# Kernel tuning notes

Measured on AMD Instinct MI355X. Metric: run time of the kernel, lower is better.

## Reference

```python
import jax, jax.numpy as jnp
import numpy as np


def setup_inputs() -> dict:
    key = jax.random.key(0)
    k1, k2 = jax.random.split(key)
    B, S, H, D = 2, 2048, 16, 64
    qk = jax.random.normal(k1, (B, S, 2, H, D), dtype=jnp.float32)
    v = jax.random.normal(k2, (B, S, H, D), dtype=jnp.float32)
    return {"qk": qk, "v": v}


def reference(qk, v):
    # qk: (B, S, 2, H, D); v: (B, S, H, D)
    seqlen = qk.shape[1]
    q = qk[:, :, 0]  # (B, S, H, D)
    k = qk[:, :, 1]
    # elu(x) + 1 feature map (positive features)
    q = jax.nn.elu(q) + 1.0
    k = jax.nn.elu(k) + 1.0
    # explicit O(S^2) score matrix: (B, H, T, S)
    scores = jnp.einsum('bthd,bshd->bhts', q, k)
    mask = jnp.tril(jnp.ones((seqlen, seqlen), dtype=scores.dtype))
    scores = scores * mask
    nu = scores.sum(axis=-1)  # (B, H, T)
    attention = scores / nu[:, :, :, None]
    # dropout_p = 0.0 (eval mode): identity
    output = jnp.einsum('bhts,bshd->bthd', attention, v)
    return output
```

## Files before the change

kernel.cpp:

```cpp
#include <hip/hip_runtime.h>


#define BB 2
#define SS 2048
#define HH 16
#define DD 64
#define CC 128
#define NC (SS / CC)
#define BH (BB * HH)
#define NCHUNK (BH * NC)

#define ST_STRIDE 8448LL
#define WS_KB (512LL * ST_STRIDE)
#define WS_VT (WS_KB + 512LL * 16384)
#define WS_S0 (WS_VT + 512LL * 16384)
#define WS_KZ (WS_S0 + 512LL * 8192)

typedef __attribute__((ext_vector_type(8))) short bf16x8;
typedef __attribute__((ext_vector_type(4))) float f32x4;

__device__ __forceinline__ float phi(float x) {
    return x > 0.f ? x + 1.f : __expf(x);
}
__device__ __forceinline__ unsigned short f2bf(float x) {
    unsigned int u = __float_as_uint(x);
    u += 0x7fffu + ((u >> 16) & 1u);
    return (unsigned short)(u >> 16);
}
__device__ __forceinline__ float bf2f(unsigned short b) {
    return __uint_as_float(((unsigned int)b) << 16);
}
__device__ __forceinline__ void gload16(const void* g, void* lds) {
    __builtin_amdgcn_global_load_lds(
        (const __attribute__((address_space(1))) unsigned int*)g,
        (__attribute__((address_space(3))) unsigned int*)lds, 16, 0, 0);
}

__global__ __launch_bounds__(256, 2)
void prep_state(const float* __restrict__ qk, const float* __restrict__ v,
                char* __restrict__ st, unsigned short* __restrict__ kbg,
                unsigned short* __restrict__ vtg) {
    __shared__ unsigned short Kt[DD][136];
    __shared__ unsigned short Vt[DD][136];

    const int tid = threadIdx.x, blk = blockIdx.x;
    const int bh = blk / NC, c = blk % NC, b = bh / HH, h = bh % HH;
    const int s0 = c * CC;
    const int lr = tid >> 4, lc = (tid & 15) * 4;
    char* kbc = (char*)kbg + (size_t)blk * 16384;

    #pragma unroll
    for (int it = 0; it < 8; ++it) {
        int row = it * 16 + lr;
        size_t ka = ((size_t)((b * SS + s0 + row) * 2 + 1)) * (HH * DD) + h * DD + lc;
        float4 kv = *(const float4*)(qk + ka);
        ushort4 kq = make_ushort4(f2bf(phi(kv.x)), f2bf(phi(kv.y)),
                                  f2bf(phi(kv.z)), f2bf(phi(kv.w)));
        *(ushort4*)(kbc + row * 128 + ((lc * 2) ^ ((row & 7) << 4))) = kq;
        Kt[lc + 0][row] = kq.x; Kt[lc + 1][row] = kq.y;
        Kt[lc + 2][row] = kq.z; Kt[lc + 3][row] = kq.w;
        size_t va = ((size_t)((b * SS + s0 + row) * HH + h)) * DD + lc;
        float4 vv = *(const float4*)(v + va);
        Vt[lc + 0][row] = f2bf(vv.x); Vt[lc + 1][row] = f2bf(vv.y);
        Vt[lc + 2][row] = f2bf(vv.z); Vt[lc + 3][row] = f2bf(vv.w);
    }
    __syncthreads();

    {
        char* vtc = (char*)vtg + (size_t)blk * 16384;
        int e = tid >> 2, sq = (tid & 3) * 32;
        #pragma unroll
        for (int k8 = 0; k8 < 4; ++k8) {
            int s = sq + k8 * 8;
            bf16x8 val = *(const bf16x8*)&Vt[e][s];
            *(bf16x8*)(vtc + e * 256 + ((s * 2) ^ ((e & 7) << 4))) = val;
        }
    }

    const int w = tid >> 6, lane = tid & 63, g = lane >> 4, ln = lane & 15;
    {
        bf16x8 av[4];
        #pragma unroll
        for (int ks = 0; ks < 4; ++ks)
            av[ks] = *(const bf16x8*)&Vt[w * 16 + ln][ks * 32 + g * 8];
        bf16x8 ones;
        #pragma unroll
        for (int j = 0; j < 8; ++j) ones[j] = (short)0x3F80;

        char* stc = st + (size_t)blk * ST_STRIDE;
        #pragma unroll
        for (int n = 0; n < 4; ++n) {
            f32x4 a = {0.f, 0.f, 0.f, 0.f}, kz4 = {0.f, 0.f, 0.f, 0.f};
            #pragma unroll
            for (int ks = 0; ks < 4; ++ks) {
                bf16x8 bk = *(const bf16x8*)&Kt[n * 16 + ln][ks * 32 + g * 8];
                a = __builtin_amdgcn_mfma_f32_16x16x32_bf16(av[ks], bk, a, 0, 0, 0);
                if (w == 0)
                    kz4 = __builtin_amdgcn_mfma_f32_16x16x32_bf16(ones, bk, kz4, 0, 0, 0);
            }
            #pragma unroll
            for (int r = 0; r < 4; ++r)
                *(unsigned short*)(stc + (((w * 16 + g * 4 + r) * 64) + n * 16 + ln) * 2)
                    = f2bf(a[r]);
            if (w == 0 && g == 0)
                *(float*)(stc + 8192 + (n * 16 + ln) * 4) = kz4[0];
        }
    }
}

__global__ __launch_bounds__(256)
void chunk_scan(const char* __restrict__ st, unsigned short* __restrict__ s0g,
                float* __restrict__ kzg) {
    int flat = blockIdx.x * 256 + threadIdx.x;
    int bh = flat / 1040, i = flat % 1040;
    const char* stb = st + (size_t)(bh * NC) * ST_STRIDE;
    if (i < 1024) {
        int i4 = i * 4, e = i4 >> 6, d = i4 & 63;
        const char* src = stb + i * 8;
        char* dst = (char*)s0g + (size_t)(bh * NC) * 8192
                    + e * 128 + ((d * 2) ^ ((e & 7) << 4));
        float4 run = {0.f, 0.f, 0.f, 0.f};
        #pragma unroll
        for (int c2 = 0; c2 < NC; ++c2) {
            *(ushort4*)(dst + (size_t)c2 * 8192) =
                make_ushort4(f2bf(run.x), f2bf(run.y), f2bf(run.z), f2bf(run.w));
            ushort4 x = *(const ushort4*)(src + (size_t)c2 * ST_STRIDE);
            run.x += bf2f(x.x); run.y += bf2f(x.y);
            run.z += bf2f(x.z); run.w += bf2f(x.w);
        }
    } else {
        int j = (i - 1024) * 4;
        const char* src = stb + 8192 + j * 4;
        float* dst = kzg + (size_t)(bh * NC) * 64 + j;
        float4 run = {0.f, 0.f, 0.f, 0.f};
        #pragma unroll
        for (int c2 = 0; c2 < NC; ++c2) {
            *(float4*)(dst + (size_t)c2 * 64) = run;
            float4 x = *(const float4*)(src + (size_t)c2 * ST_STRIDE);
            run.x += x.x; run.y += x.y; run.z += x.z; run.w += x.w;
        }
    }
}

__global__ __launch_bounds__(256, 2)
void lin_attn_out(const float* __restrict__ qk,
                  const unsigned short* __restrict__ kbg,
                  const unsigned short* __restrict__ vtg,
                  const unsigned short* __restrict__ s0g,
                  const float* __restrict__ kzg,
                  float* __restrict__ out) {
    __shared__ __align__(16) char KbL[16384];
    __shared__ __align__(16) char VtL[16384];
    __shared__ __align__(16) char S0L[8192];
    __shared__ float kzl[DD];
    __shared__ __align__(16) unsigned short Wl[4][32][40];
    __shared__ float nul[4][32];

    const int tid = threadIdx.x, blk = blockIdx.x;
    const int bh = blk / NC, c = blk % NC, b = bh / HH, h = bh % HH;
    const int s0 = c * CC;
    const int w = tid >> 6, lane = tid & 63, g = lane >> 4, ln = lane & 15;
    const int wband = (blk & 1) ? (3 - w) : w;

    {
        const char* kbs = (const char*)kbg + (size_t)blk * 16384;
        const char* vts = (const char*)vtg + (size_t)blk * 16384;
        const char* s0s = (const char*)s0g + (size_t)blk * 8192;
        #pragma unroll
        for (int i = 0; i < 4; ++i) {
            gload16(kbs + w * 4096 + i * 1024 + lane * 16, KbL + w * 4096 + i * 1024);
            gload16(vts + w * 4096 + i * 1024 + lane * 16, VtL + w * 4096 + i * 1024);
        }
        #pragma unroll
        for (int i = 0; i < 2; ++i)
            gload16(s0s + w * 2048 + i * 1024 + lane * 16, S0L + w * 2048 + i * 1024);
        if (tid < DD) kzl[tid] = kzg[(size_t)blk * 64 + tid];
    }

    bf16x8 aq[2][2];
    #pragma unroll
    for (int m = 0; m < 2; ++m) {
        int tg = s0 + wband * 32 + m * 16 + ln;
        const float* qrow = qk + ((size_t)((b * SS + tg) * 2)) * (HH * DD) + h * DD;
        #pragma unroll
        for (int kb2 = 0; kb2 < 2; ++kb2) {
            float4 x0 = *(const float4*)(qrow + kb2 * 32 + g * 8);
            float4 x1 = *(const float4*)(qrow + kb2 * 32 + g * 8 + 4);
            bf16x8 f;
            f[0] = (short)f2bf(phi(x0.x)); f[1] = (short)f2bf(phi(x0.y));
            f[2] = (short)f2bf(phi(x0.z)); f[3] = (short)f2bf(phi(x0.w));
            f[4] = (short)f2bf(phi(x1.x)); f[5] = (short)f2bf(phi(x1.y));
            f[6] = (short)f2bf(phi(x1.z)); f[7] = (short)f2bf(phi(x1.w));
            aq[m][kb2] = f;
        }
    }
    __syncthreads();

    f32x4 O[2][4];
    #pragma unroll
    for (int m = 0; m < 2; ++m)
        #pragma unroll
        for (int n = 0; n < 4; ++n) O[m][n] = (f32x4){0.f, 0.f, 0.f, 0.f};

    #pragma unroll
    for (int n = 0; n < 4; ++n) {
        int e = n * 16 + ln;
        bf16x8 b0 = *(const bf16x8*)(S0L + e * 128 + ((g * 16) ^ ((e & 7) << 4)));
        bf16x8 b1 = *(const bf16x8*)(S0L + e * 128 + ((64 + g * 16) ^ ((e & 7) << 4)));
        #pragma unroll
        for (int m = 0; m < 2; ++m) {
            O[m][n] = __builtin_amdgcn_mfma_f32_16x16x32_bf16(aq[m][0], b0, O[m][n], 0, 0, 0);
            O[m][n] = __builtin_amdgcn_mfma_f32_16x16x32_bf16(aq[m][1], b1, O[m][n], 0, 0, 0);
        }
    }

    float nuA[2] = {0.f, 0.f};
    #pragma unroll
    for (int kb2 = 0; kb2 < 2; ++kb2)
        #pragma unroll
        for (int j = 0; j < 8; ++j) {
            float kzv = kzl[kb2 * 32 + g * 8 + j];
            nuA[0] = fmaf(bf2f((unsigned short)aq[0][kb2][j]), kzv, nuA[0]);
            nuA[1] = fmaf(bf2f((unsigned short)aq[1][kb2][j]), kzv, nuA[1]);
        }

    for (int sblk = 0; sblk <= wband; ++sblk) {
        const bool diag = (sblk == wband);
        f32x4 Sc[2][2];
        #pragma unroll
        for (int m = 0; m < 2; ++m)
            #pragma unroll
            for (int ns = 0; ns < 2; ++ns) Sc[m][ns] = (f32x4){0.f, 0.f, 0.f, 0.f};

        #pragma unroll
        for (int ns = 0; ns < 2; ++ns) {
            int s = sblk * 32 + ns * 16 + ln;
            const char* srow = KbL + s * 128;
            bf16x8 bk0 = *(const bf16x8*)(srow + ((g * 16) ^ ((s & 7) << 4)));
            bf16x8 bk1 = *(const bf16x8*)(srow + ((64 + g * 16) ^ ((s & 7) << 4)));
            #pragma unroll
            for (int m = 0; m < 2; ++m) {
                Sc[m][ns] = __builtin_amdgcn_mfma_f32_16x16x32_bf16(aq[m][0], bk0, Sc[m][ns], 0, 0, 0);
                Sc[m][ns] = __builtin_amdgcn_mfma_f32_16x16x32_bf16(aq[m][1], bk1, Sc[m][ns], 0, 0, 0);
            }
        }

        #pragma unroll
        for (int m = 0; m < 2; ++m)
            #pragma unroll
            for (int ns = 0; ns < 2; ++ns)
                #pragma unroll
                for (int r = 0; r < 4; ++r) {
                    int t_loc = m * 16 + g * 4 + r;
                    int s_loc = ns * 16 + ln;
                    float val = Sc[m][ns][r];
                    if (diag && s_loc > t_loc) val = 0.f;
                    Wl[w][t_loc][s_loc] = f2bf(val);
                }
        asm volatile("s_waitcnt lgkmcnt(0)" ::: "memory");
        __builtin_amdgcn_sched_barrier(0);

        bf16x8 bv[4];
        #pragma unroll
        for (int n = 0; n < 4; ++n) {
            int e = n * 16 + ln;
            bv[n] = *(const bf16x8*)(VtL + e * 256 + ((sblk * 64 + g * 16) ^ ((e & 7) << 4)));
        }

        #pragma unroll
        for (int m = 0; m < 2; ++m) {
            bf16x8 pa = *(const bf16x8*)&Wl[w][m * 16 + ln][g * 8];
            float rs = 0.f;
            #pragma unroll
            for (int j = 0; j < 8; ++j) rs += bf2f((unsigned short)pa[j]);
            nuA[m] += rs;
            #pragma unroll
            for (int n = 0; n < 4; ++n)
                O[m][n] = __builtin_amdgcn_mfma_f32_16x16x32_bf16(pa, bv[n], O[m][n], 0, 0, 0);
        }
    }

    #pragma unroll
    for (int m = 0; m < 2; ++m) {
        float nt = nuA[m];
        nt += __shfl_xor(nt, 16);
        nt += __shfl_xor(nt, 32);
        if (g == 0) nul[w][m * 16 + ln] = nt;
    }
    asm volatile("s_waitcnt lgkmcnt(0)" ::: "memory");
    __builtin_amdgcn_sched_barrier(0);

    #pragma unroll
    for (int m = 0; m < 2; ++m) {
        float inv[4];
        #pragma unroll
        for (int r = 0; r < 4; ++r) inv[r] = 1.f / nul[w][m * 16 + g * 4 + r];
        #pragma unroll
        for (int n = 0; n < 4; ++n)
            #pragma unroll
            for (int r = 0; r < 4; ++r) {
                int t = wband * 32 + m * 16 + g * 4 + r;
                int e = n * 16 + ln;
                size_t oa = ((size_t)((b * SS + s0 + t) * HH + h)) * DD + e;
                out[oa] = O[m][n][r] * inv[r];
            }
    }
}

extern "C" void kernel_launch(void* const* d_in, const int* in_sizes, int n_in,
                              void* d_out, int out_size, void* d_ws, size_t ws_size,
                              hipStream_t stream) {
    const float* qk = (const float*)d_in[0];
    const float* v  = (const float*)d_in[1];
    float* outp = (float*)d_out;

    char* st = (char*)d_ws;
    unsigned short* kbg = (unsigned short*)((char*)d_ws + WS_KB);
    unsigned short* vtg = (unsigned short*)((char*)d_ws + WS_VT);
    unsigned short* s0g = (unsigned short*)((char*)d_ws + WS_S0);
    float* kzg = (float*)((char*)d_ws + WS_KZ);

    prep_state<<<NCHUNK, 256, 0, stream>>>(qk, v, st, kbg, vtg);
    chunk_scan<<<130, 256, 0, stream>>>(st, s0g, kzg);
    lin_attn_out<<<NCHUNK, 256, 0, stream>>>(qk, kbg, vtg, s0g, kzg, outp);
}
```

Measured before the change: 34.00 us.

## Fuse chunk prefix scan into output kernel and keep scores in registers

Removes the separate chunk_scan kernel: each output block now sums the per-chunk states of all preceding chunks itself, building S0 and kz directly in shared memory. The score tile is computed transposed, masked, and row-summed in registers, then redistributed into the MFMA A-operand layout with lane shuffles instead of a round trip through an LDS staging buffer. This saves one kernel launch and the LDS write/read/wait per score block. In exchange, later chunks redundantly read and accumulate up to 15 chunk states, which makes work across blocks uneven.

Measured after the change: 37.56 us. 1.1x slower.

```diff
diff --git a/kernel.cpp b/kernel.cpp
--- a/kernel.cpp
+++ b/kernel.cpp
@@ -13,8 +13,6 @@
 #define ST_STRIDE 8448LL
 #define WS_KB (512LL * ST_STRIDE)
 #define WS_VT (WS_KB + 512LL * 16384)
-#define WS_S0 (WS_VT + 512LL * 16384)
-#define WS_KZ (WS_S0 + 512LL * 8192)
 
 typedef __attribute__((ext_vector_type(8))) short bf16x8;
 typedef __attribute__((ext_vector_type(4))) float f32x4;
@@ -108,52 +106,16 @@
     }
 }
 
-__global__ __launch_bounds__(256)
-void chunk_scan(const char* __restrict__ st, unsigned short* __restrict__ s0g,
-                float* __restrict__ kzg) {
-    int flat = blockIdx.x * 256 + threadIdx.x;
-    int bh = flat / 1040, i = flat % 1040;
-    const char* stb = st + (size_t)(bh * NC) * ST_STRIDE;
-    if (i < 1024) {
-        int i4 = i * 4, e = i4 >> 6, d = i4 & 63;
-        const char* src = stb + i * 8;
-        char* dst = (char*)s0g + (size_t)(bh * NC) * 8192
-                    + e * 128 + ((d * 2) ^ ((e & 7) << 4));
-        float4 run = {0.f, 0.f, 0.f, 0.f};
-        #pragma unroll
-        for (int c2 = 0; c2 < NC; ++c2) {
-            *(ushort4*)(dst + (size_t)c2 * 8192) =
-                make_ushort4(f2bf(run.x), f2bf(run.y), f2bf(run.z), f2bf(run.w));
-            ushort4 x = *(const ushort4*)(src + (size_t)c2 * ST_STRIDE);
-            run.x += bf2f(x.x); run.y += bf2f(x.y);
-            run.z += bf2f(x.z); run.w += bf2f(x.w);
-        }
-    } else {
-        int j = (i - 1024) * 4;
-        const char* src = stb + 8192 + j * 4;
-        float* dst = kzg + (size_t)(bh * NC) * 64 + j;
-        float4 run = {0.f, 0.f, 0.f, 0.f};
-        #pragma unroll
-        for (int c2 = 0; c2 < NC; ++c2) {
-            *(float4*)(dst + (size_t)c2 * 64) = run;
-            float4 x = *(const float4*)(src + (size_t)c2 * ST_STRIDE);
-            run.x += x.x; run.y += x.y; run.z += x.z; run.w += x.w;
-        }
-    }
-}
-
 __global__ __launch_bounds__(256, 2)
 void lin_attn_out(const float* __restrict__ qk,
                   const unsigned short* __restrict__ kbg,
                   const unsigned short* __restrict__ vtg,
-                  const unsigned short* __restrict__ s0g,
-                  const float* __restrict__ kzg,
+                  const char* __restrict__ st,
                   float* __restrict__ out) {
     __shared__ __align__(16) char KbL[16384];
     __shared__ __align__(16) char VtL[16384];
     __shared__ __align__(16) char S0L[8192];
     __shared__ float kzl[DD];
-    __shared__ __align__(16) unsigned short Wl[4][32][40];
     __shared__ float nul[4][32];
 
     const int tid = threadIdx.x, blk = blockIdx.x;
@@ -165,16 +127,44 @@
     {
         const char* kbs = (const char*)kbg + (size_t)blk * 16384;
         const char* vts = (const char*)vtg + (size_t)blk * 16384;
-        const char* s0s = (const char*)s0g + (size_t)blk * 8192;
         #pragma unroll
         for (int i = 0; i < 4; ++i) {
             gload16(kbs + w * 4096 + i * 1024 + lane * 16, KbL + w * 4096 + i * 1024);
             gload16(vts + w * 4096 + i * 1024 + lane * 16, VtL + w * 4096 + i * 1024);
         }
-        #pragma unroll
-        for (int i = 0; i < 2; ++i)
-            gload16(s0s + w * 2048 + i * 1024 + lane * 16, S0L + w * 2048 + i * 1024);
-        if (tid < DD) kzl[tid] = kzg[(size_t)blk * 64 + tid];
+    }
+
+    {
+        const char* stb = st + (size_t)(bh * NC) * ST_STRIDE;
+        float acc[16];
+        #pragma unroll
+        for (int j = 0; j < 16; ++j) acc[j] = 0.f;
+        for (int c2 = 0; c2 < c; ++c2) {
+            const char* src = stb + (size_t)c2 * ST_STRIDE + tid * 32;
+            bf16x8 x0 = *(const bf16x8*)src;
+            bf16x8 x1 = *(const bf16x8*)(src + 16);
+            #pragma unroll
+            for (int j = 0; j < 8; ++j) {
+                acc[j]     += bf2f((unsigned short)x0[j]);
+                acc[j + 8] += bf2f((unsigned short)x1[j]);
+            }
+        }
+        int e = tid >> 2, d0 = (tid & 3) * 16;
+        bf16x8 o0, o1;
+        #pragma unroll
+        for (int j = 0; j < 8; ++j) {
+            o0[j] = (short)f2bf(acc[j]);
+            o1[j] = (short)f2bf(acc[j + 8]);
+        }
+        int sw = (e & 7) << 4;
+        *(bf16x8*)(S0L + e * 128 + ((2 * d0) ^ sw)) = o0;
+        *(bf16x8*)(S0L + e * 128 + ((2 * d0 + 16) ^ sw)) = o1;
+        if (tid < DD) {
+            float a = 0.f;
+            for (int c2 = 0; c2 < c; ++c2)
+                a += *(const float*)(stb + (size_t)c2 * ST_STRIDE + 8192 + 4 * tid);
+            kzl[tid] = a;
+        }
     }
 
     bf16x8 aq[2][2];
@@ -224,13 +214,15 @@
             nuA[1] = fmaf(bf2f((unsigned short)aq[1][kb2][j]), kzv, nuA[1]);
         }
 
+    const int srcA = ((lane & 16) << 1) + ln;
+    const bool hiT = (lane & 32) != 0;
     for (int sblk = 0; sblk <= wband; ++sblk) {
         const bool diag = (sblk == wband);
-        f32x4 Sc[2][2];
+        f32x4 ScT[2][2];
         #pragma unroll
         for (int m = 0; m < 2; ++m)
             #pragma unroll
-            for (int ns = 0; ns < 2; ++ns) Sc[m][ns] = (f32x4){0.f, 0.f, 0.f, 0.f};
+            for (int ns = 0; ns < 2; ++ns) ScT[m][ns] = (f32x4){0.f, 0.f, 0.f, 0.f};
 
         #pragma unroll
         for (int ns = 0; ns < 2; ++ns) {
@@ -240,8 +232,8 @@
             bf16x8 bk1 = *(const bf16x8*)(srow + ((64 + g * 16) ^ ((s & 7) << 4)));
             #pragma unroll
             for (int m = 0; m < 2; ++m) {
-                Sc[m][ns] = __builtin_amdgcn_mfma_f32_16x16x32_bf16(aq[m][0], bk0, Sc[m][ns], 0, 0, 0);
-                Sc[m][ns] = __builtin_amdgcn_mfma_f32_16x16x32_bf16(aq[m][1], bk1, Sc[m][ns], 0, 0, 0);
+                ScT[m][ns] = __builtin_amdgcn_mfma_f32_16x16x32_bf16(bk0, aq[m][0], ScT[m][ns], 0, 0, 0);
+                ScT[m][ns] = __builtin_amdgcn_mfma_f32_16x16x32_bf16(bk1, aq[m][1], ScT[m][ns], 0, 0, 0);
             }
         }
 
@@ -251,14 +243,10 @@
             for (int ns = 0; ns < 2; ++ns)
                 #pragma unroll
                 for (int r = 0; r < 4; ++r) {
-                    int t_loc = m * 16 + g * 4 + r;
-                    int s_loc = ns * 16 + ln;
-                    float val = Sc[m][ns][r];
-                    if (diag && s_loc > t_loc) val = 0.f;
-                    Wl[w][t_loc][s_loc] = f2bf(val);
+                    if (diag && (ns * 16 + g * 4 + r > m * 16 + ln))
+                        ScT[m][ns][r] = 0.f;
+                    nuA[m] += ScT[m][ns][r];
                 }
-        asm volatile("s_waitcnt lgkmcnt(0)" ::: "memory");
-        __builtin_amdgcn_sched_barrier(0);
 
         bf16x8 bv[4];
         #pragma unroll
@@ -269,11 +257,14 @@
 
         #pragma unroll
         for (int m = 0; m < 2; ++m) {
-            bf16x8 pa = *(const bf16x8*)&Wl[w][m * 16 + ln][g * 8];
-            float rs = 0.f;
-            #pragma unroll
-            for (int j = 0; j < 8; ++j) rs += bf2f((unsigned short)pa[j]);
-            nuA[m] += rs;
+            bf16x8 pa;
+            #pragma unroll
+            for (int j = 0; j < 8; ++j) {
+                int sl = (j < 4) ? srcA : (srcA + 16);
+                float v0 = __shfl(ScT[m][0][j & 3], sl);
+                float v1 = __shfl(ScT[m][1][j & 3], sl);
+                pa[j] = (short)f2bf(hiT ? v1 : v0);
+            }
             #pragma unroll
             for (int n = 0; n < 4; ++n)
                 O[m][n] = __builtin_amdgcn_mfma_f32_16x16x32_bf16(pa, bv[n], O[m][n], 0, 0, 0);
@@ -317,10 +308,7 @@
     char* st = (char*)d_ws;
     unsigned short* kbg = (unsigned short*)((char*)d_ws + WS_KB);
     unsigned short* vtg = (unsigned short*)((char*)d_ws + WS_VT);
-    unsigned short* s0g = (unsigned short*)((char*)d_ws + WS_S0);
-    float* kzg = (float*)((char*)d_ws + WS_KZ);
 
     prep_state<<<NCHUNK, 256, 0, stream>>>(qk, v, st, kbg, vtg);
-    chunk_scan<<<130, 256, 0, stream>>>(st, s0g, kzg);
-    lin_attn_out<<<NCHUNK, 256, 0, stream>>>(qk, kbg, vtg, s0g, kzg, outp);
-}
+    lin_attn_out<<<NCHUNK, 256, 0, stream>>>(qk, kbg, vtg, st, outp);
+}
```

## Halve chunk size to 64 for intra-chunk attention, reducing quadratic work

Applied to the files above, without the earlier changes.

Each block of 128 rows now holds two 64-row sub-chunks, and the prep kernel writes a separate partial state per sub-chunk. The scan therefore runs over 32 sub-chunks per head, and each wave does causal attention over at most 64 keys instead of 128, which cuts the diagonal quadratic work. The cost is twice as much state written, scanned and loaded, a longer serial scan, more LDS, and a change to occupancy hints. The wave band mapping and the W-tile padding were also changed.

After: 37.41 us. 10.0% more time.

```diff
diff --git a/kernel.cpp b/kernel.cpp
--- a/kernel.cpp
+++ b/kernel.cpp
@@ -5,18 +5,16 @@
 #define SS 2048
 #define HH 16
 #define DD 64
-#define CC 128
-#define NC (SS / CC)
-#define BH (BB * HH)
-#define NCHUNK (BH * NC)
-
-#define ST_STRIDE 8448LL
-#define WS_KB (512LL * ST_STRIDE)
+#define NBLK 512
+#define ST64 8448LL
+
+#define WS_KB (1024LL * ST64)
 #define WS_VT (WS_KB + 512LL * 16384)
 #define WS_S0 (WS_VT + 512LL * 16384)
-#define WS_KZ (WS_S0 + 512LL * 8192)
+#define WS_KZ (WS_S0 + 1024LL * 8192)
 
 typedef __attribute__((ext_vector_type(8))) short bf16x8;
+typedef __attribute__((ext_vector_type(4))) short bf16x4;
 typedef __attribute__((ext_vector_type(4))) float f32x4;
 
 __device__ __forceinline__ float phi(float x) {
@@ -36,7 +34,7 @@
         (__attribute__((address_space(3))) unsigned int*)lds, 16, 0, 0);
 }
 
-__global__ __launch_bounds__(256, 2)
+__global__ __launch_bounds__(256, 4)
 void prep_state(const float* __restrict__ qk, const float* __restrict__ v,
                 char* __restrict__ st, unsigned short* __restrict__ kbg,
                 unsigned short* __restrict__ vtg) {
@@ -44,8 +42,8 @@
     __shared__ unsigned short Vt[DD][136];
 
     const int tid = threadIdx.x, blk = blockIdx.x;
-    const int bh = blk / NC, c = blk % NC, b = bh / HH, h = bh % HH;
-    const int s0 = c * CC;
+    const int bh = blk >> 4, j = blk & 15, b = bh / HH, h = bh % HH;
+    const int s0 = j * 128;
     const int lr = tid >> 4, lc = (tid & 15) * 4;
     char* kbc = (char*)kbg + (size_t)blk * 16384;
 
@@ -85,25 +83,38 @@
             av[ks] = *(const bf16x8*)&Vt[w * 16 + ln][ks * 32 + g * 8];
         bf16x8 ones;
         #pragma unroll
-        for (int j = 0; j < 8; ++j) ones[j] = (short)0x3F80;
-
-        char* stc = st + (size_t)blk * ST_STRIDE;
+        for (int jj = 0; jj < 8; ++jj) ones[jj] = (short)0x3F80;
+
+        char* stc0 = st + (size_t)(blk * 2 + 0) * ST64;
+        char* stc1 = st + (size_t)(blk * 2 + 1) * ST64;
         #pragma unroll
         for (int n = 0; n < 4; ++n) {
-            f32x4 a = {0.f, 0.f, 0.f, 0.f}, kz4 = {0.f, 0.f, 0.f, 0.f};
-            #pragma unroll
-            for (int ks = 0; ks < 4; ++ks) {
-                bf16x8 bk = *(const bf16x8*)&Kt[n * 16 + ln][ks * 32 + g * 8];
-                a = __builtin_amdgcn_mfma_f32_16x16x32_bf16(av[ks], bk, a, 0, 0, 0);
-                if (w == 0)
-                    kz4 = __builtin_amdgcn_mfma_f32_16x16x32_bf16(ones, bk, kz4, 0, 0, 0);
-            }
-            #pragma unroll
-            for (int r = 0; r < 4; ++r)
-                *(unsigned short*)(stc + (((w * 16 + g * 4 + r) * 64) + n * 16 + ln) * 2)
-                    = f2bf(a[r]);
-            if (w == 0 && g == 0)
-                *(float*)(stc + 8192 + (n * 16 + ln) * 4) = kz4[0];
+            f32x4 aA = {0.f, 0.f, 0.f, 0.f}, aB = {0.f, 0.f, 0.f, 0.f};
+            f32x4 kzA = {0.f, 0.f, 0.f, 0.f}, kzB = {0.f, 0.f, 0.f, 0.f};
+            bf16x8 bk0 = *(const bf16x8*)&Kt[n * 16 + ln][0 * 32 + g * 8];
+            bf16x8 bk1 = *(const bf16x8*)&Kt[n * 16 + ln][1 * 32 + g * 8];
+            bf16x8 bk2 = *(const bf16x8*)&Kt[n * 16 + ln][2 * 32 + g * 8];
+            bf16x8 bk3 = *(const bf16x8*)&Kt[n * 16 + ln][3 * 32 + g * 8];
+            aA = __builtin_amdgcn_mfma_f32_16x16x32_bf16(av[0], bk0, aA, 0, 0, 0);
+            aA = __builtin_amdgcn_mfma_f32_16x16x32_bf16(av[1], bk1, aA, 0, 0, 0);
+            aB = __builtin_amdgcn_mfma_f32_16x16x32_bf16(av[2], bk2, aB, 0, 0, 0);
+            aB = __builtin_amdgcn_mfma_f32_16x16x32_bf16(av[3], bk3, aB, 0, 0, 0);
+            if (w == 0) {
+                kzA = __builtin_amdgcn_mfma_f32_16x16x32_bf16(ones, bk0, kzA, 0, 0, 0);
+                kzA = __builtin_amdgcn_mfma_f32_16x16x32_bf16(ones, bk1, kzA, 0, 0, 0);
+                kzB = __builtin_amdgcn_mfma_f32_16x16x32_bf16(ones, bk2, kzB, 0, 0, 0);
+                kzB = __builtin_amdgcn_mfma_f32_16x16x32_bf16(ones, bk3, kzB, 0, 0, 0);
+            }
+            #pragma unroll
+            for (int r = 0; r < 4; ++r) {
+                int off = (((w * 16 + g * 4 + r) * 64) + n * 16 + ln) * 2;
+                *(unsigned short*)(stc0 + off) = f2bf(aA[r]);
+                *(unsigned short*)(stc1 + off) = f2bf(aB[r]);
+            }
+            if (w == 0 && g == 0) {
+                *(float*)(stc0 + 8192 + (n * 16 + ln) * 4) = kzA[0];
+                *(float*)(stc1 + 8192 + (n * 16 + ln) * 4) = kzB[0];
+            }
         }
     }
 }
@@ -113,30 +124,30 @@
                 float* __restrict__ kzg) {
     int flat = blockIdx.x * 256 + threadIdx.x;
     int bh = flat / 1040, i = flat % 1040;
-    const char* stb = st + (size_t)(bh * NC) * ST_STRIDE;
+    const char* stb = st + (size_t)(bh * 32) * ST64;
     if (i < 1024) {
         int i4 = i * 4, e = i4 >> 6, d = i4 & 63;
         const char* src = stb + i * 8;
-        char* dst = (char*)s0g + (size_t)(bh * NC) * 8192
+        char* dst = (char*)s0g + (size_t)(bh * 32) * 8192
                     + e * 128 + ((d * 2) ^ ((e & 7) << 4));
         float4 run = {0.f, 0.f, 0.f, 0.f};
         #pragma unroll
-        for (int c2 = 0; c2 < NC; ++c2) {
-            *(ushort4*)(dst + (size_t)c2 * 8192) =
+        for (int cc = 0; cc < 32; ++cc) {
+            *(ushort4*)(dst + (size_t)cc * 8192) =
                 make_ushort4(f2bf(run.x), f2bf(run.y), f2bf(run.z), f2bf(run.w));
-            ushort4 x = *(const ushort4*)(src + (size_t)c2 * ST_STRIDE);
+            ushort4 x = *(const ushort4*)(src + (size_t)cc * ST64);
             run.x += bf2f(x.x); run.y += bf2f(x.y);
             run.z += bf2f(x.z); run.w += bf2f(x.w);
         }
     } else {
-        int j = (i - 1024) * 4;
-        const char* src = stb + 8192 + j * 4;
-        float* dst = kzg + (size_t)(bh * NC) * 64 + j;
+        int jj = (i - 1024) * 4;
+        const char* src = stb + 8192 + jj * 4;
+        float* dst = kzg + (size_t)(bh * 32) * 64 + jj;
         float4 run = {0.f, 0.f, 0.f, 0.f};
         #pragma unroll
-        for (int c2 = 0; c2 < NC; ++c2) {
-            *(float4*)(dst + (size_t)c2 * 64) = run;
-            float4 x = *(const float4*)(src + (size_t)c2 * ST_STRIDE);
+        for (int cc = 0; cc < 32; ++cc) {
+            *(float4*)(dst + (size_t)cc * 64) = run;
+            float4 x = *(const float4*)(src + (size_t)cc * ST64);
             run.x += x.x; run.y += x.y; run.z += x.z; run.w += x.w;
         }
     }
@@ -151,36 +162,36 @@
                   float* __restrict__ out) {
     __shared__ __align__(16) char KbL[16384];
     __shared__ __align__(16) char VtL[16384];
-    __shared__ __align__(16) char S0L[8192];
-    __shared__ float kzl[DD];
-    __shared__ __align__(16) unsigned short Wl[4][32][40];
+    __shared__ __align__(16) char S0L[16384];
+    __shared__ float kzl[128];
+    __shared__ __align__(16) unsigned short Wl[4][32][44];
     __shared__ float nul[4][32];
 
     const int tid = threadIdx.x, blk = blockIdx.x;
-    const int bh = blk / NC, c = blk % NC, b = bh / HH, h = bh % HH;
-    const int s0 = c * CC;
+    const int bh = blk >> 4, j = blk & 15, b = bh / HH, h = bh % HH;
+    const int rb = j * 128;
     const int w = tid >> 6, lane = tid & 63, g = lane >> 4, ln = lane & 15;
-    const int wband = (blk & 1) ? (3 - w) : w;
+    const int flip = (blk >> 8) & 1;
+    const int ch = w >> 1;
+    const int bnd = (w & 1) ^ flip;
 
     {
         const char* kbs = (const char*)kbg + (size_t)blk * 16384;
         const char* vts = (const char*)vtg + (size_t)blk * 16384;
-        const char* s0s = (const char*)s0g + (size_t)blk * 8192;
+        const char* s0s = (const char*)s0g + (size_t)(bh * 32 + j * 2) * 8192;
         #pragma unroll
         for (int i = 0; i < 4; ++i) {
             gload16(kbs + w * 4096 + i * 1024 + lane * 16, KbL + w * 4096 + i * 1024);
             gload16(vts + w * 4096 + i * 1024 + lane * 16, VtL + w * 4096 + i * 1024);
-        }
-        #pragma unroll
-        for (int i = 0; i < 2; ++i)
-            gload16(s0s + w * 2048 + i * 1024 + lane * 16, S0L + w * 2048 + i * 1024);
-        if (tid < DD) kzl[tid] = kzg[(size_t)blk * 64 + tid];
+            gload16(s0s + w * 4096 + i * 1024 + lane * 16, S0L + w * 4096 + i * 1024);
+        }
+        if (tid < 128) kzl[tid] = kzg[(size_t)(bh * 32 + j * 2) * 64 + tid];
     }
 
     bf16x8 aq[2][2];
     #pragma unroll
     for (int m = 0; m < 2; ++m) {
-        int tg = s0 + wband * 32 + m * 16 + ln;
+        int tg = rb + ch * 64 + bnd * 32 + m * 16 + ln;
         const float* qrow = qk + ((size_t)((b * SS + tg) * 2)) * (HH * DD) + h * DD;
         #pragma unroll
         for (int kb2 = 0; kb2 < 2; ++kb2) {
@@ -202,11 +213,12 @@
         #pragma unroll
         for (int n = 0; n < 4; ++n) O[m][n] = (f32x4){0.f, 0.f, 0.f, 0.f};
 
+    const char* S0c = S0L + ch * 8192;
     #pragma unroll
     for (int n = 0; n < 4; ++n) {
         int e = n * 16 + ln;
-        bf16x8 b0 = *(const bf16x8*)(S0L + e * 128 + ((g * 16) ^ ((e & 7) << 4)));
-        bf16x8 b1 = *(const bf16x8*)(S0L + e * 128 + ((64 + g * 16) ^ ((e & 7) << 4)));
+        bf16x8 b0 = *(const bf16x8*)(S0c + e * 128 + ((g * 16) ^ ((e & 7) << 4)));
+        bf16x8 b1 = *(const bf16x8*)(S0c + e * 128 + ((64 + g * 16) ^ ((e & 7) << 4)));
         #pragma unroll
         for (int m = 0; m < 2; ++m) {
             O[m][n] = __builtin_amdgcn_mfma_f32_16x16x32_bf16(aq[m][0], b0, O[m][n], 0, 0, 0);
@@ -218,14 +230,14 @@
     #pragma unroll
     for (int kb2 = 0; kb2 < 2; ++kb2)
         #pragma unroll
-        for (int j = 0; j < 8; ++j) {
-            float kzv = kzl[kb2 * 32 + g * 8 + j];
-            nuA[0] = fmaf(bf2f((unsigned short)aq[0][kb2][j]), kzv, nuA[0]);
-            nuA[1] = fmaf(bf2f((unsigned short)aq[1][kb2][j]), kzv, nuA[1]);
-        }
-
-    for (int sblk = 0; sblk <= wband; ++sblk) {
-        const bool diag = (sblk == wband);
+        for (int jj = 0; jj < 8; ++jj) {
+            float kzv = kzl[ch * 64 + kb2 * 32 + g * 8 + jj];
+            nuA[0] = fmaf(bf2f((unsigned short)aq[0][kb2][jj]), kzv, nuA[0]);
+            nuA[1] = fmaf(bf2f((unsigned short)aq[1][kb2][jj]), kzv, nuA[1]);
+        }
+
+    for (int sblk = 0; sblk <= bnd; ++sblk) {
+        const bool diag = (sblk == bnd);
         f32x4 Sc[2][2];
         #pragma unroll
         for (int m = 0; m < 2; ++m)
@@ -234,7 +246,7 @@
 
         #pragma unroll
         for (int ns = 0; ns < 2; ++ns) {
-            int s = sblk * 32 + ns * 16 + ln;
+            int s = ch * 64 + sblk * 32 + ns * 16 + ln;
             const char* srow = KbL + s * 128;
             bf16x8 bk0 = *(const bf16x8*)(srow + ((g * 16) ^ ((s & 7) << 4)));
             bf16x8 bk1 = *(const bf16x8*)(srow + ((64 + g * 16) ^ ((s & 7) << 4)));
@@ -264,15 +276,19 @@
         #pragma unroll
         for (int n = 0; n < 4; ++n) {
             int e = n * 16 + ln;
-            bv[n] = *(const bf16x8*)(VtL + e * 256 + ((sblk * 64 + g * 16) ^ ((e & 7) << 4)));
+            bv[n] = *(const bf16x8*)(VtL + e * 256
+                        + ((((ch * 2 + sblk) * 64) + g * 16) ^ ((e & 7) << 4)));
         }
 
         #pragma unroll
         for (int m = 0; m < 2; ++m) {
-            bf16x8 pa = *(const bf16x8*)&Wl[w][m * 16 + ln][g * 8];
+            const unsigned short* prow = &Wl[w][m * 16 + ln][0];
+            bf16x4 plo = *(const bf16x4*)(prow + g * 8);
+            bf16x4 phi2 = *(const bf16x4*)(prow + g * 8 + 4);
+            bf16x8 pa = __builtin_shufflevector(plo, phi2, 0, 1, 2, 3, 4, 5, 6, 7);
             float rs = 0.f;
             #pragma unroll
-            for (int j = 0; j < 8; ++j) rs += bf2f((unsigned short)pa[j]);
+            for (int jj = 0; jj < 8; ++jj) rs += bf2f((unsigned short)pa[jj]);
             nuA[m] += rs;
             #pragma unroll
             for (int n = 0; n < 4; ++n)
@@ -299,9 +315,9 @@
         for (int n = 0; n < 4; ++n)
             #pragma unroll
             for (int r = 0; r < 4; ++r) {
-                int t = wband * 32 + m * 16 + g * 4 + r;
+                int t = ch * 64 + bnd * 32 + m * 16 + g * 4 + r;
                 int e = n * 16 + ln;
-                size_t oa = ((size_t)((b * SS + s0 + t) * HH + h)) * DD + e;
+                size_t oa = ((size_t)((b * SS + rb + t) * HH + h)) * DD + e;
                 out[oa] = O[m][n][r] * inv[r];
             }
     }
@@ -320,7 +336,7 @@
     unsigned short* s0g = (unsigned short*)((char*)d_ws + WS_S0);
     float* kzg = (float*)((char*)d_ws + WS_KZ);
 
-    prep_state<<<NCHUNK, 256, 0, stream>>>(qk, v, st, kbg, vtg);
+    prep_state<<<NBLK, 256, 0, stream>>>(qk, v, st, kbg, vtg);
     chunk_scan<<<130, 256, 0, stream>>>(st, s0g, kzg);
-    lin_attn_out<<<NCHUNK, 256, 0, stream>>>(qk, kbg, vtg, s0g, kzg, outp);
-}
+    lin_attn_out<<<NBLK, 256, 0, stream>>>(qk, kbg, vtg, s0g, kzg, outp);
+}
```
